# Optimization experiments

Hardware: AMD Instinct MI355X
Metric: run time of the kernel (lower is better)

The kernel has to match this reference:

```python
import jax, jax.numpy as jnp
import numpy as np


def _pick(key, nodes, mask, cnt):
    # Uniformly pick one of the `cnt` entries of `nodes` where mask is True.
    r = jax.random.randint(key, (), 0, jnp.maximum(cnt, 1))
    cs = jnp.cumsum(mask.astype(jnp.int32))
    return nodes[jnp.argmax(cs == r + 1)]


def _one_walk(key, nbrs, f0, n_faces, L):
    # nbrs: [N,3] int32 neighbor table, f0: scalar start face.
    seq = jnp.zeros((L + 1,), jnp.int32).at[0].set(f0)
    visited = jnp.zeros((n_faces + 1,), bool).at[n_faces].set(True).at[f0].set(True)

    def cond(st):
        return st[2] <= L

    def body(st):
        seq, visited, i, bs, k = st
        k, k1, k2, k3 = jax.random.split(k, 4)
        cur = seq[i - 1]
        nb = nbrs[cur]                     # [3] neighbor candidates
        unv = ~visited[nb]
        cnt = unv.sum()
        need = cnt == 0                    # stuck -> backtrack
        cand = _pick(k1, nb, unv, cnt)

        def bcond(c):
            bs_c, found = c[0], c[1]
            return need & (~found) & (i > bs_c)

        def bbody(c):
            bs_c, found, ta, kk = c
            kk, kp = jax.random.split(kk)
            back = seq[i - bs_c - 1]
            bn = nbrs[back]
            bm = ~visited[bn]
            bc = bm.sum()
            f2 = bc > 0
            ta2 = _pick(kp, bn, bm, bc)
            return (jnp.where(f2, bs_c, bs_c + 2), f2, jnp.where(f2, ta2, ta), kk)

        bs_f, found, ta_bt, _ = jax.lax.while_loop(
            bcond, bbody, (bs, jnp.array(False), jnp.int32(0), k2))
        rand_node = jax.random.randint(k3, (), 0, n_faces, dtype=jnp.int32)
        to_add = jnp.where(~need, cand, jnp.where(found, ta_bt, rand_node))
        hit = need & found                 # successful backtrack
        bs_new = jnp.where(hit, bs_f, jnp.int32(1))
        i_new = jnp.where(hit, i - bs_f, i)
        ar = jnp.arange(L + 1, dtype=jnp.int32)
        # torch: replace seq[i-bs:i] with to_add on successful backtrack
        seq = jnp.where(hit & (ar >= i_new) & (ar < i), to_add, seq)
        visited = visited.at[to_add].set(True)
        seq = seq.at[i_new].set(to_add)
        return (seq, visited, i_new + 1, bs_new, k)

    seq, *_ = jax.lax.while_loop(
        cond, body, (seq, visited, jnp.int32(1), jnp.int32(1), key))
    return seq


def patch_random_walk(key, neighbors, centers, n_faces, seq_len):
    B, G = centers.shape
    keys = jax.random.split(key, B * G).reshape(B, G)
    walk_g = jax.vmap(_one_walk, in_axes=(0, None, 0, None, None))
    walk_bg = jax.vmap(walk_g, in_axes=(0, 0, 0, None, None))
    return walk_bg(keys, neighbors, centers, n_faces, seq_len)  # [B,G,L+1] int32


def setup_inputs() -> dict:
    key = jax.random.key(0)
    k1, k2, k3 = jax.random.split(key, 3)
    B, N, G = 4, 20000, 1024
    xyz = jax.random.normal(k1, (B, N, 3), dtype=jnp.float32)
    neighbors = jax.random.randint(k2, (B, N, 3), 0, N, dtype=jnp.int32)
    centers = jax.random.randint(k3, (B, G), 0, N, dtype=jnp.int32)
    return {"xyz": xyz, "neighbors": neighbors, "centers": centers,
            "n_faces": N, "seq_len": 63}


def reference(xyz, neighbors, centers, n_faces, seq_len):
    # patch_random_walk -> idx [B,G,K]; then Group.forward gather + recenter.
    idx = patch_random_walk(jax.random.key(42), neighbors, centers, n_faces, seq_len)
    gather = jax.vmap(lambda p, i: p[i])(xyz, idx)            # [B,G,K,3]
    center_xyz = jax.vmap(lambda p, c: p[c])(xyz, centers)    # [B,G,3]
    return gather - center_xyz[:, :, None, :]
```

## Files before the change

kernel.cpp:

```cpp
#include <hip/hip_runtime.h>
#include <stdint.h>
#include <stddef.h>


namespace {

__device__ __forceinline__ uint32_t rotl32(uint32_t x, int r) {
  return (x << r) | (x >> (32 - r));
}

__device__ __forceinline__ void tf2x32(uint32_t ka, uint32_t kb,
                                       uint32_t x0, uint32_t x1,
                                       uint32_t& o0, uint32_t& o1) {
  const uint32_t kc = ka ^ kb ^ 0x1BD11BDAu;
  x0 += ka; x1 += kb;
#define TF_R4(r0, r1, r2, r3)                          \
  x0 += x1; x1 = rotl32(x1, r0); x1 ^= x0;             \
  x0 += x1; x1 = rotl32(x1, r1); x1 ^= x0;             \
  x0 += x1; x1 = rotl32(x1, r2); x1 ^= x0;             \
  x0 += x1; x1 = rotl32(x1, r3); x1 ^= x0;
  TF_R4(13, 15, 26, 6)  x0 += kb; x1 += kc + 1u;
  TF_R4(17, 29, 16, 24) x0 += kc; x1 += ka + 2u;
  TF_R4(13, 15, 26, 6)  x0 += ka; x1 += kb + 3u;
  TF_R4(17, 29, 16, 24) x0 += kb; x1 += kc + 4u;
  TF_R4(13, 15, 26, 6)  x0 += kc; x1 += ka + 5u;
#undef TF_R4
  o0 = x0; o1 = x1;
}

__device__ __forceinline__ void randbits(uint32_t ka, uint32_t kb,
                                         uint32_t& hi, uint32_t& lo) {
  uint32_t s0a, s0b, s1a, s1b, h0, h1;
  tf2x32(ka, kb, 0u, 0u, s0a, s0b);
  tf2x32(ka, kb, 0u, 1u, s1a, s1b);
  tf2x32(s0a, s0b, 0u, 0u, h0, h1);
  hi = h0 ^ h1;
  tf2x32(s1a, s1b, 0u, 0u, h0, h1);
  lo = h0 ^ h1;
}

__device__ __forceinline__ uint32_t r_generic(uint32_t hi, uint32_t lo,
                                              uint32_t span) {
  uint32_t mult = 65536u % span;
  mult = (mult * mult) % span;
  return ((hi % span) * mult + (lo % span)) % span;
}

__device__ __forceinline__ uint32_t pick_code(uint32_t hi, uint32_t lo) {
  return ((hi % 3u + lo % 3u) % 3u) | ((lo & 1u) << 2);
}

constexpr int WPB = 16;
constexpr int CH = 64;

__global__ __launch_bounds__(1024) void walk_kernel(
    const float* __restrict__ xyz, const int* __restrict__ nbrs,
    const int* __restrict__ centers, const int* __restrict__ n_faces_p,
    const int* __restrict__ seq_len_p, float* __restrict__ out,
    int s0, int num_walks, int Lp1) {
  __shared__ uint2 keys[WPB][CH + 1];
  __shared__ uint32_t pre[WPB][CH];

  const int tid = threadIdx.x;
  const int wv = tid >> 6, lane = tid & 63;
  const int w0 = blockIdx.x * WPB;
  const int w = w0 + wv;
  const bool active = (w < num_walks);

  const int N = *n_faces_p;
  const int L = *seq_len_p;
  const int B = s0 / (3 * N);
  const int G = num_walks / B;
  const int b = (active ? w : w0) / G;
  const int* __restrict__ nb  = nbrs + (size_t)b * N * 3;
  const float* __restrict__ xb = xyz + (size_t)b * N * 3;

  int f0 = 0;
  int3 row = make_int3(0, 0, 0);
  if (active) {
    f0 = centers[w];
    row = *reinterpret_cast<const int3*>(nb + 3 * (size_t)f0);
  }

  if (wv == 0) {
    if (lane < WPB && (w0 + lane) < num_walks) {
      uint32_t ka, kb;
      tf2x32(0u, 42u, 0u, (uint32_t)(w0 + lane), ka, kb);
      keys[lane][0] = make_uint2(ka, kb);
#pragma clang loop unroll(disable)
      for (int c = 1; c < CH; ++c) {
        tf2x32(ka, kb, 0u, 0u, ka, kb);
        keys[lane][c] = make_uint2(ka, kb);
      }
    }
  } else {
    const int nq = (N * 3) >> 2;
    const int j0 = tid - 64;
    const int4* __restrict__ pn = reinterpret_cast<const int4*>(nb);
    const int4* __restrict__ px = reinterpret_cast<const int4*>(xb);
    int acc = 0;
    for (int j = j0; j < nq; j += 960) {
      const int4 a = pn[j];
      const int4 c4 = px[j];
      acc ^= a.x ^ a.y ^ a.z ^ a.w ^ c4.x ^ c4.y ^ c4.z ^ c4.w;
    }
    asm volatile("" :: "v"(acc));
  }
  __syncthreads();
  if (!active) return;

  int3 t0 = *reinterpret_cast<const int3*>(nb + 3 * (size_t)row.x);
  int3 t1 = *reinterpret_cast<const int3*>(nb + 3 * (size_t)row.y);
  int3 t2 = *reinterpret_cast<const int3*>(nb + 3 * (size_t)row.z);

  {
    const uint2 kc = keys[wv][lane];
    uint32_t k1a, k1b, hi, lo;
    tf2x32(kc.x, kc.y, 0u, 1u, k1a, k1b);
    randbits(k1a, k1b, hi, lo);
    pre[wv][lane] = pick_code(hi, lo);
  }

  int hist  = (lane == 0) ? f0 : -1;
  int hist2 = -1;
  int seqr  = (lane == 0) ? f0 : -1;

  uint32_t extka = 0, extkb = 0;
  int extc = -1;

  auto get_key = [&](int idx, uint32_t& ra, uint32_t& rb) {
    if (idx < CH) {
      const uint2 q = keys[wv][idx]; ra = q.x; rb = q.y;
    } else {
      if (extc < 0) { const uint2 q = keys[wv][CH - 1]; extka = q.x; extkb = q.y; extc = CH - 1; }
      while (extc < idx) { tf2x32(extka, extkb, 0u, 0u, extka, extkb); ++extc; }
      ra = extka; rb = extkb;
    }
  };

  uint32_t code_next = pre[wv][0];
  int i = 1, bs = 1, c = 0;

  while (i <= L) {
    const int idx = c; ++c;
    const bool deep = (idx >= CH);
    const uint32_t codeP = code_next;
    code_next = pre[wv][(c < CH) ? c : 0];

    const int n0 = row.x, n1 = row.y, n2 = row.z;
    int v0 = __any(hist == n0), v1 = __any(hist == n1), v2 = __any(hist == n2);
    if (deep) {
      v0 |= __any(hist2 == n0); v1 |= __any(hist2 == n1); v2 |= __any(hist2 == n2);
    }
    const int u0 = 1 - v0, u1 = 1 - v1, u2 = 1 - v2;
    const int cnt = u0 + u1 + u2;

    int to_add;
    int sel = -1;
    bool hit = false;
    int bsf = bs;
    if (cnt > 0) {
      uint32_t code;
      if (!deep) {
        code = codeP;
      } else {
        uint32_t ia, ib, k1a, k1b, hi, lo;
        get_key(idx, ia, ib);
        tf2x32(ia, ib, 0u, 1u, k1a, k1b);
        randbits(k1a, k1b, hi, lo);
        code = pick_code(hi, lo);
      }
      const int r3 = (int)(code & 3u), r2 = (int)((code >> 2) & 1u);
      const int target = (cnt == 3 ? r3 : (cnt == 2 ? r2 : 0)) + 1;
      sel = (u0 == target) ? 0 : ((u0 + u1 == target) ? 1 : 2);
      to_add = (sel == 0) ? n0 : ((sel == 1) ? n1 : n2);
    } else {
      uint32_t kia, kib;
      get_key(idx, kia, kib);
      uint32_t kka, kkb;
      tf2x32(kia, kib, 0u, 2u, kka, kkb);
      bool found = false;
      int ta = 0, bsc = bs;
      while (!found && i > bsc) {
        uint32_t ca, cb, kpa, kpb;
        tf2x32(kka, kkb, 0u, 0u, ca, cb);
        tf2x32(kka, kkb, 0u, 1u, kpa, kpb);
        const int back = __shfl(seqr, i - bsc - 1);
        const int3 br = *reinterpret_cast<const int3*>(nb + 3 * (size_t)back);
        int w0m = __any(hist == br.x), w1m = __any(hist == br.y), w2m = __any(hist == br.z);
        if (deep) {
          w0m |= __any(hist2 == br.x); w1m |= __any(hist2 == br.y); w2m |= __any(hist2 == br.z);
        }
        const int e0 = 1 - w0m, e1 = 1 - w1m, e2 = 1 - w2m;
        const int bc = e0 + e1 + e2;
        if (bc > 0) {
          uint32_t bhi, blo;
          randbits(kpa, kpb, bhi, blo);
          const uint32_t bcode = pick_code(bhi, blo);
          const int r3 = (int)(bcode & 3u), r2 = (int)((bcode >> 2) & 1u);
          const int t2v = (bc == 3 ? r3 : (bc == 2 ? r2 : 0)) + 1;
          ta = (e0 == t2v) ? br.x : ((e0 + e1 == t2v) ? br.y : br.z);
          found = true;
        } else {
          bsc += 2;
        }
        kka = ca; kkb = cb;
      }
      if (found) {
        to_add = ta; hit = true; bsf = bsc;
      } else {
        uint32_t k3a, k3b, rhi, rlo;
        tf2x32(kia, kib, 0u, 3u, k3a, k3b);
        randbits(k3a, k3b, rhi, rlo);
        to_add = (int)r_generic(rhi, rlo, (uint32_t)N);
      }
    }

    int i_new, up;
    if (hit) { i_new = i - bsf; bs = bsf; up = i - 1; }
    else     { i_new = i;       bs = 1;   up = i; }
    seqr = (lane >= i_new && lane <= up) ? to_add : seqr;

    const int slot = idx + 1;
    if (slot < CH)            hist  = (lane == slot)      ? to_add : hist;
    else if (slot < 2 * CH)   hist2 = (lane == slot - CH) ? to_add : hist2;

    i = i_new + 1;

    if (sel >= 0) {
      row.x = (sel == 0) ? t0.x : ((sel == 1) ? t1.x : t2.x);
      row.y = (sel == 0) ? t0.y : ((sel == 1) ? t1.y : t2.y);
      row.z = (sel == 0) ? t0.z : ((sel == 1) ? t1.z : t2.z);
    } else {
      row = *reinterpret_cast<const int3*>(nb + 3 * (size_t)to_add);
    }
    t0 = *reinterpret_cast<const int3*>(nb + 3 * (size_t)row.x);
    t1 = *reinterpret_cast<const int3*>(nb + 3 * (size_t)row.y);
    t2 = *reinterpret_cast<const int3*>(nb + 3 * (size_t)row.z);
  }

  const float cx = xb[3 * (size_t)f0 + 0];
  const float cy = xb[3 * (size_t)f0 + 1];
  const float cz = xb[3 * (size_t)f0 + 2];
  if (lane < Lp1) {
    const int node = seqr;
    float3 v;
    v.x = xb[3 * (size_t)node + 0] - cx;
    v.y = xb[3 * (size_t)node + 1] - cy;
    v.z = xb[3 * (size_t)node + 2] - cz;
    *reinterpret_cast<float3*>(out + ((size_t)w * Lp1 + lane) * 3) = v;
  }
}

}

extern "C" void kernel_launch(void* const* d_in, const int* in_sizes, int n_in,
                              void* d_out, int out_size, void* d_ws, size_t ws_size,
                              hipStream_t stream) {
  const float* xyz     = (const float*)d_in[0];
  const int*   nbrs    = (const int*)d_in[1];
  const int*   centers = (const int*)d_in[2];
  const int*   n_faces = (const int*)d_in[3];
  const int*   seq_len = (const int*)d_in[4];
  float* out = (float*)d_out;

  const int s0 = in_sizes[0];
  const int num_walks = in_sizes[2];
  const int Lp1 = out_size / (3 * num_walks);

  const int blocks = (num_walks + WPB - 1) / WPB;
  walk_kernel<<<blocks, WPB * 64, 0, stream>>>(
      xyz, nbrs, centers, n_faces, seq_len, out, s0, num_walks, Lp1);
}
```

Measured before the change: 106.8 us.

## Split key generation into separate kernel and pass keys via registers and shuffles

```diff
diff --git a/kernel.cpp b/kernel.cpp
--- a/kernel.cpp
+++ b/kernel.cpp
@@ -50,77 +50,69 @@
   return ((hi % 3u + lo % 3u) % 3u) | ((lo & 1u) << 2);
 }
 
-constexpr int WPB = 16;
 constexpr int CH = 64;
-
-__global__ __launch_bounds__(1024) void walk_kernel(
+constexpr int K1_WPB = 16;
+constexpr int K2_WPB = 4;
+
+__global__ __launch_bounds__(1024) void keys_kernel(
+    uint2* __restrict__ keys_g, uint32_t* __restrict__ codes_g,
+    int num_walks) {
+  __shared__ uint2 keys[K1_WPB][CH + 1];
+
+  const int tid = threadIdx.x;
+  const int wv = tid >> 6, lane = tid & 63;
+  const int w0 = blockIdx.x * K1_WPB;
+  const int w = w0 + wv;
+
+  if (wv == 0 && lane < K1_WPB && (w0 + lane) < num_walks) {
+    uint32_t ka, kb;
+    tf2x32(0u, 42u, 0u, (uint32_t)(w0 + lane), ka, kb);
+    keys[lane][0] = make_uint2(ka, kb);
+#pragma clang loop unroll(disable)
+    for (int c = 1; c < CH; ++c) {
+      tf2x32(ka, kb, 0u, 0u, ka, kb);
+      keys[lane][c] = make_uint2(ka, kb);
+    }
+  }
+  __syncthreads();
+  if (w >= num_walks) return;
+
+  const uint2 kc = keys[wv][lane];
+  uint32_t k1a, k1b, hi, lo;
+  tf2x32(kc.x, kc.y, 0u, 1u, k1a, k1b);
+  randbits(k1a, k1b, hi, lo);
+  keys_g[(size_t)w * CH + lane]  = kc;
+  codes_g[(size_t)w * CH + lane] = pick_code(hi, lo);
+}
+
+__global__ __launch_bounds__(256) void walk_kernel(
     const float* __restrict__ xyz, const int* __restrict__ nbrs,
     const int* __restrict__ centers, const int* __restrict__ n_faces_p,
     const int* __restrict__ seq_len_p, float* __restrict__ out,
+    const uint2* __restrict__ keys_g, const uint32_t* __restrict__ codes_g,
     int s0, int num_walks, int Lp1) {
-  __shared__ uint2 keys[WPB][CH + 1];
-  __shared__ uint32_t pre[WPB][CH];
-
   const int tid = threadIdx.x;
   const int wv = tid >> 6, lane = tid & 63;
-  const int w0 = blockIdx.x * WPB;
-  const int w = w0 + wv;
-  const bool active = (w < num_walks);
+  const int w = blockIdx.x * K2_WPB + wv;
+  if (w >= num_walks) return;
 
   const int N = *n_faces_p;
   const int L = *seq_len_p;
   const int B = s0 / (3 * N);
   const int G = num_walks / B;
-  const int b = (active ? w : w0) / G;
-  const int* __restrict__ nb  = nbrs + (size_t)b * N * 3;
+  const int b = w / G;
+  const int* __restrict__ nb   = nbrs + (size_t)b * N * 3;
   const float* __restrict__ xb = xyz + (size_t)b * N * 3;
 
-  int f0 = 0;
-  int3 row = make_int3(0, 0, 0);
-  if (active) {
-    f0 = centers[w];
-    row = *reinterpret_cast<const int3*>(nb + 3 * (size_t)f0);
-  }
-
-  if (wv == 0) {
-    if (lane < WPB && (w0 + lane) < num_walks) {
-      uint32_t ka, kb;
-      tf2x32(0u, 42u, 0u, (uint32_t)(w0 + lane), ka, kb);
-      keys[lane][0] = make_uint2(ka, kb);
-#pragma clang loop unroll(disable)
-      for (int c = 1; c < CH; ++c) {
-        tf2x32(ka, kb, 0u, 0u, ka, kb);
-        keys[lane][c] = make_uint2(ka, kb);
-      }
-    }
-  } else {
-    const int nq = (N * 3) >> 2;
-    const int j0 = tid - 64;
-    const int4* __restrict__ pn = reinterpret_cast<const int4*>(nb);
-    const int4* __restrict__ px = reinterpret_cast<const int4*>(xb);
-    int acc = 0;
-    for (int j = j0; j < nq; j += 960) {
-      const int4 a = pn[j];
-      const int4 c4 = px[j];
-      acc ^= a.x ^ a.y ^ a.z ^ a.w ^ c4.x ^ c4.y ^ c4.z ^ c4.w;
-    }
-    asm volatile("" :: "v"(acc));
-  }
-  __syncthreads();
-  if (!active) return;
-
+  const uint2 mykey = keys_g[(size_t)w * CH + lane];
+  const uint32_t mycode = codes_g[(size_t)w * CH + lane];
+
+  const int f0 = centers[w];
+  int3 row = *reinterpret_cast<const int3*>(nb + 3 * (size_t)f0);
   int3 t0 = *reinterpret_cast<const int3*>(nb + 3 * (size_t)row.x);
   int3 t1 = *reinterpret_cast<const int3*>(nb + 3 * (size_t)row.y);
   int3 t2 = *reinterpret_cast<const int3*>(nb + 3 * (size_t)row.z);
 
-  {
-    const uint2 kc = keys[wv][lane];
-    uint32_t k1a, k1b, hi, lo;
-    tf2x32(kc.x, kc.y, 0u, 1u, k1a, k1b);
-    randbits(k1a, k1b, hi, lo);
-    pre[wv][lane] = pick_code(hi, lo);
-  }
-
   int hist  = (lane == 0) ? f0 : -1;
   int hist2 = -1;
   int seqr  = (lane == 0) ? f0 : -1;
@@ -130,22 +122,27 @@
 
   auto get_key = [&](int idx, uint32_t& ra, uint32_t& rb) {
     if (idx < CH) {
-      const uint2 q = keys[wv][idx]; ra = q.x; rb = q.y;
-    } else {
-      if (extc < 0) { const uint2 q = keys[wv][CH - 1]; extka = q.x; extkb = q.y; extc = CH - 1; }
+      ra = (uint32_t)__shfl((int)mykey.x, idx);
+      rb = (uint32_t)__shfl((int)mykey.y, idx);
+    } else {
+      if (extc < 0) {
+        extka = (uint32_t)__shfl((int)mykey.x, CH - 1);
+        extkb = (uint32_t)__shfl((int)mykey.y, CH - 1);
+        extc = CH - 1;
+      }
       while (extc < idx) { tf2x32(extka, extkb, 0u, 0u, extka, extkb); ++extc; }
       ra = extka; rb = extkb;
     }
   };
 
-  uint32_t code_next = pre[wv][0];
+  uint32_t code_next = (uint32_t)__shfl((int)mycode, 0);
   int i = 1, bs = 1, c = 0;
 
   while (i <= L) {
     const int idx = c; ++c;
     const bool deep = (idx >= CH);
     const uint32_t codeP = code_next;
-    code_next = pre[wv][(c < CH) ? c : 0];
+    code_next = (uint32_t)__shfl((int)mycode, (c < CH) ? c : 0);
 
     const int n0 = row.x, n1 = row.y, n2 = row.z;
     int v0 = __any(hist == n0), v1 = __any(hist == n1), v2 = __any(hist == n2);
@@ -252,6 +249,191 @@
   }
 }
 
+__global__ __launch_bounds__(1024) void fused_kernel(
+    const float* __restrict__ xyz, const int* __restrict__ nbrs,
+    const int* __restrict__ centers, const int* __restrict__ n_faces_p,
+    const int* __restrict__ seq_len_p, float* __restrict__ out,
+    int s0, int num_walks, int Lp1) {
+  __shared__ uint2 keys[K1_WPB][CH + 1];
+  __shared__ uint32_t pre[K1_WPB][CH];
+
+  const int tid = threadIdx.x;
+  const int wv = tid >> 6, lane = tid & 63;
+  const int w0 = blockIdx.x * K1_WPB;
+  const int w = w0 + wv;
+  const bool active = (w < num_walks);
+
+  const int N = *n_faces_p;
+  const int L = *seq_len_p;
+  const int B = s0 / (3 * N);
+  const int G = num_walks / B;
+  const int b = (active ? w : w0) / G;
+  const int* __restrict__ nb   = nbrs + (size_t)b * N * 3;
+  const float* __restrict__ xb = xyz + (size_t)b * N * 3;
+
+  int f0 = 0;
+  int3 row = make_int3(0, 0, 0);
+  if (active) {
+    f0 = centers[w];
+    row = *reinterpret_cast<const int3*>(nb + 3 * (size_t)f0);
+  }
+
+  if (wv == 0 && lane < K1_WPB && (w0 + lane) < num_walks) {
+    uint32_t ka, kb;
+    tf2x32(0u, 42u, 0u, (uint32_t)(w0 + lane), ka, kb);
+    keys[lane][0] = make_uint2(ka, kb);
+#pragma clang loop unroll(disable)
+    for (int c = 1; c < CH; ++c) {
+      tf2x32(ka, kb, 0u, 0u, ka, kb);
+      keys[lane][c] = make_uint2(ka, kb);
+    }
+  }
+  __syncthreads();
+  if (!active) return;
+
+  int3 t0 = *reinterpret_cast<const int3*>(nb + 3 * (size_t)row.x);
+  int3 t1 = *reinterpret_cast<const int3*>(nb + 3 * (size_t)row.y);
+  int3 t2 = *reinterpret_cast<const int3*>(nb + 3 * (size_t)row.z);
+
+  {
+    const uint2 kc = keys[wv][lane];
+    uint32_t k1a, k1b, hi, lo;
+    tf2x32(kc.x, kc.y, 0u, 1u, k1a, k1b);
+    randbits(k1a, k1b, hi, lo);
+    pre[wv][lane] = pick_code(hi, lo);
+  }
+
+  int hist  = (lane == 0) ? f0 : -1;
+  int hist2 = -1;
+  int seqr  = (lane == 0) ? f0 : -1;
+
+  uint32_t extka = 0, extkb = 0;
+  int extc = -1;
+
+  auto get_key = [&](int idx, uint32_t& ra, uint32_t& rb) {
+    if (idx < CH) {
+      const uint2 q = keys[wv][idx]; ra = q.x; rb = q.y;
+    } else {
+      if (extc < 0) { const uint2 q = keys[wv][CH - 1]; extka = q.x; extkb = q.y; extc = CH - 1; }
+      while (extc < idx) { tf2x32(extka, extkb, 0u, 0u, extka, extkb); ++extc; }
+      ra = extka; rb = extkb;
+    }
+  };
+
+  uint32_t code_next = pre[wv][0];
+  int i = 1, bs = 1, c = 0;
+
+  while (i <= L) {
+    const int idx = c; ++c;
+    const bool deep = (idx >= CH);
+    const uint32_t codeP = code_next;
+    code_next = pre[wv][(c < CH) ? c : 0];
+
+    const int n0 = row.x, n1 = row.y, n2 = row.z;
+    int v0 = __any(hist == n0), v1 = __any(hist == n1), v2 = __any(hist == n2);
+    if (deep) {
+      v0 |= __any(hist2 == n0); v1 |= __any(hist2 == n1); v2 |= __any(hist2 == n2);
+    }
+    const int u0 = 1 - v0, u1 = 1 - v1, u2 = 1 - v2;
+    const int cnt = u0 + u1 + u2;
+
+    int to_add;
+    int sel = -1;
+    bool hit = false;
+    int bsf = bs;
+    if (cnt > 0) {
+      uint32_t code;
+      if (!deep) {
+        code = codeP;
+      } else {
+        uint32_t ia, ib, k1a, k1b, hi, lo;
+        get_key(idx, ia, ib);
+        tf2x32(ia, ib, 0u, 1u, k1a, k1b);
+        randbits(k1a, k1b, hi, lo);
+        code = pick_code(hi, lo);
+      }
+      const int r3 = (int)(code & 3u), r2 = (int)((code >> 2) & 1u);
+      const int target = (cnt == 3 ? r3 : (cnt == 2 ? r2 : 0)) + 1;
+      sel = (u0 == target) ? 0 : ((u0 + u1 == target) ? 1 : 2);
+      to_add = (sel == 0) ? n0 : ((sel == 1) ? n1 : n2);
+    } else {
+      uint32_t kia, kib;
+      get_key(idx, kia, kib);
+      uint32_t kka, kkb;
+      tf2x32(kia, kib, 0u, 2u, kka, kkb);
+      bool found = false;
+      int ta = 0, bsc = bs;
+      while (!found && i > bsc) {
+        uint32_t ca, cb, kpa, kpb;
+        tf2x32(kka, kkb, 0u, 0u, ca, cb);
+        tf2x32(kka, kkb, 0u, 1u, kpa, kpb);
+        const int back = __shfl(seqr, i - bsc - 1);
+        const int3 br = *reinterpret_cast<const int3*>(nb + 3 * (size_t)back);
+        int w0m = __any(hist == br.x), w1m = __any(hist == br.y), w2m = __any(hist == br.z);
+        if (deep) {
+          w0m |= __any(hist2 == br.x); w1m |= __any(hist2 == br.y); w2m |= __any(hist2 == br.z);
+        }
+        const int e0 = 1 - w0m, e1 = 1 - w1m, e2 = 1 - w2m;
+        const int bc = e0 + e1 + e2;
+        if (bc > 0) {
+          uint32_t bhi, blo;
+          randbits(kpa, kpb, bhi, blo);
+          const uint32_t bcode = pick_code(bhi, blo);
+          const int r3 = (int)(bcode & 3u), r2 = (int)((bcode >> 2) & 1u);
+          const int t2v = (bc == 3 ? r3 : (bc == 2 ? r2 : 0)) + 1;
+          ta = (e0 == t2v) ? br.x : ((e0 + e1 == t2v) ? br.y : br.z);
+          found = true;
+        } else {
+          bsc += 2;
+        }
+        kka = ca; kkb = cb;
+      }
+      if (found) {
+        to_add = ta; hit = true; bsf = bsc;
+      } else {
+        uint32_t k3a, k3b, rhi, rlo;
+        tf2x32(kia, kib, 0u, 3u, k3a, k3b);
+        randbits(k3a, k3b, rhi, rlo);
+        to_add = (int)r_generic(rhi, rlo, (uint32_t)N);
+      }
+    }
+
+    int i_new, up;
+    if (hit) { i_new = i - bsf; bs = bsf; up = i - 1; }
+    else     { i_new = i;       bs = 1;   up = i; }
+    seqr = (lane >= i_new && lane <= up) ? to_add : seqr;
+
+    const int slot = idx + 1;
+    if (slot < CH)            hist  = (lane == slot)      ? to_add : hist;
+    else if (slot < 2 * CH)   hist2 = (lane == slot - CH) ? to_add : hist2;
+
+    i = i_new + 1;
+
+    if (sel >= 0) {
+      row.x = (sel == 0) ? t0.x : ((sel == 1) ? t1.x : t2.x);
+      row.y = (sel == 0) ? t0.y : ((sel == 1) ? t1.y : t2.y);
+      row.z = (sel == 0) ? t0.z : ((sel == 1) ? t1.z : t2.z);
+    } else {
+      row = *reinterpret_cast<const int3*>(nb + 3 * (size_t)to_add);
+    }
+    t0 = *reinterpret_cast<const int3*>(nb + 3 * (size_t)row.x);
+    t1 = *reinterpret_cast<const int3*>(nb + 3 * (size_t)row.y);
+    t2 = *reinterpret_cast<const int3*>(nb + 3 * (size_t)row.z);
+  }
+
+  const float cx = xb[3 * (size_t)f0 + 0];
+  const float cy = xb[3 * (size_t)f0 + 1];
+  const float cz = xb[3 * (size_t)f0 + 2];
+  if (lane < Lp1) {
+    const int node = seqr;
+    float3 v;
+    v.x = xb[3 * (size_t)node + 0] - cx;
+    v.y = xb[3 * (size_t)node + 1] - cy;
+    v.z = xb[3 * (size_t)node + 2] - cz;
+    *reinterpret_cast<float3*>(out + ((size_t)w * Lp1 + lane) * 3) = v;
+  }
+}
+
 }
 
 extern "C" void kernel_launch(void* const* d_in, const int* in_sizes, int n_in,
@@ -268,7 +450,23 @@
   const int num_walks = in_sizes[2];
   const int Lp1 = out_size / (3 * num_walks);
 
-  const int blocks = (num_walks + WPB - 1) / WPB;
-  walk_kernel<<<blocks, WPB * 64, 0, stream>>>(
-      xyz, nbrs, centers, n_faces, seq_len, out, s0, num_walks, Lp1);
-}
+  const size_t keys_bytes  = (size_t)num_walks * CH * sizeof(uint2);
+  const size_t codes_bytes = (size_t)num_walks * CH * sizeof(uint32_t);
+
+  if (ws_size >= keys_bytes + codes_bytes) {
+    uint2*    keys_g  = (uint2*)d_ws;
+    uint32_t* codes_g = (uint32_t*)((char*)d_ws + keys_bytes);
+
+    const int blocks1 = (num_walks + K1_WPB - 1) / K1_WPB;
+    keys_kernel<<<blocks1, K1_WPB * 64, 0, stream>>>(keys_g, codes_g, num_walks);
+
+    const int blocks2 = (num_walks + K2_WPB - 1) / K2_WPB;
+    walk_kernel<<<blocks2, K2_WPB * 64, 0, stream>>>(
+        xyz, nbrs, centers, n_faces, seq_len, out, keys_g, codes_g,
+        s0, num_walks, Lp1);
+  } else {
+    const int blocks = (num_walks + K1_WPB - 1) / K1_WPB;
+    fused_kernel<<<blocks, K1_WPB * 64, 0, stream>>>(
+        xyz, nbrs, centers, n_faces, seq_len, out, s0, num_walks, Lp1);
+  }
+}
```

New measurement: 112.9 us. 5.7% more time.
